# Performance work log

Measured on AMD Instinct MI355X. Metric: run time of the kernel, lower is better.

## Reference

```python
import jax, jax.numpy as jnp
import numpy as np

NQ, NS, D, NUM_CLASSES = 8192, 16384, 512, 64


def setup_inputs() -> dict:
    key = jax.random.key(0)
    k1, k2, k3 = jax.random.split(key, 3)
    query_embeddings = jax.random.normal(k1, (NQ, D), dtype=jnp.float32)
    support_embeddings = jax.random.normal(k2, (NS, D), dtype=jnp.float32)
    # one-hot support labels [NS, NUM_CLASSES]
    labels = jax.random.randint(k3, (NS,), 0, NUM_CLASSES)
    support_labels_onehot = jax.nn.one_hot(labels, NUM_CLASSES, dtype=jnp.float32)
    return {
        "query_embeddings": query_embeddings,
        "support_embeddings": support_embeddings,
        "support_labels_onehot": support_labels_onehot,
    }


def reference(query_embeddings, support_embeddings, support_labels_onehot):
    """KNNLearner.predict_prob with distance_type='cosine'.

    distance = -cos_sim(query, support)          [NQ, NS]
    top-1 over (-distance) -> nearest support, value = max similarity
    gather support label, one-hot, scale by value. [NQ, NUM_CLASSES]
    """
    eps = 1e-12  # tf.nn.l2_normalize epsilon guard
    q = query_embeddings * jax.lax.rsqrt(
        jnp.maximum(jnp.sum(query_embeddings * query_embeddings, axis=1, keepdims=True), eps))
    s = support_embeddings * jax.lax.rsqrt(
        jnp.maximum(jnp.sum(support_embeddings * support_embeddings, axis=1, keepdims=True), eps))
    distance = -jnp.einsum('qd,sd->qs', q, s)  # [NQ, NS]
    values, indices = jax.lax.top_k(-distance, 1)  # [NQ,1], similarity of nearest neighbor
    indices = indices[:, 0]
    values = values[:, 0]
    labels_x = jnp.argmax(support_labels_onehot, axis=1)  # [NS]
    labels_pred = labels_x[indices]  # [NQ]
    num_classes = support_labels_onehot.shape[1]
    labels_onehot = jax.nn.one_hot(labels_pred, num_classes, dtype=values.dtype)
    labels_prob = labels_onehot * values[:, None]  # [NQ, NUM_CLASSES]
    return labels_prob
```

## Files before the change

### kernel.cpp

```cpp
#include <hip/hip_runtime.h>
#include <stdint.h>

#define NQ 8192
#define NS 16384
#define DIM 512
#define NC 64
#define MARGIN 0.01f
#define CAND_CAP (1 << 20)
#define LCAP 1024

typedef unsigned short ushort;
typedef __attribute__((ext_vector_type(8))) short bf16x8;
typedef __attribute__((ext_vector_type(4))) float f32x4;

__device__ __forceinline__ uint32_t fkey(float f) {
  uint32_t u = __float_as_uint(f);
  return (u & 0x80000000u) ? ~u : (u | 0x80000000u);
}
__device__ __forceinline__ float unfkey(uint32_t k) {
  return __uint_as_float((k & 0x80000000u) ? (k & 0x7FFFFFFFu) : ~k);
}
__device__ __forceinline__ ushort f2bf_rne(float f) {
  uint32_t u = __float_as_uint(f);
  return (ushort)((u + 0x7fffu + ((u >> 16) & 1u)) >> 16);
}
__device__ __forceinline__ void gload_lds16(const void* g, void* lds) {
  __builtin_amdgcn_global_load_lds(
      (const __attribute__((address_space(1))) uint32_t*)g,
      (__attribute__((address_space(3))) uint32_t*)lds, 16, 0, 0);
}

__global__ void norm_bf16_kernel(const float* __restrict__ X,
                                 ushort* __restrict__ Xbf, float* __restrict__ rX,
                                 int nrows) {
  int w = threadIdx.x >> 6, l = threadIdx.x & 63;
  int row = blockIdx.x * 4 + w;
  if (row >= nrows) return;
  const float4* x = (const float4*)(X + (size_t)row * DIM);
  float4 v0 = x[l], v1 = x[l + 64];
  float s = v0.x*v0.x + v0.y*v0.y + v0.z*v0.z + v0.w*v0.w
          + v1.x*v1.x + v1.y*v1.y + v1.z*v1.z + v1.w*v1.w;
  #pragma unroll
  for (int off = 32; off; off >>= 1) s += __shfl_xor(s, off);
  float r = rsqrtf(fmaxf(s, 1e-12f));
  if (l == 0) rX[row] = r;
  size_t base = (size_t)row * DIM + 4 * l;
  *(ushort4*)&Xbf[base] = make_ushort4(f2bf_rne(v0.x*r), f2bf_rne(v0.y*r),
                                       f2bf_rne(v0.z*r), f2bf_rne(v0.w*r));
  *(ushort4*)&Xbf[base + 256] = make_ushort4(f2bf_rne(v1.x*r), f2bf_rne(v1.y*r),
                                             f2bf_rne(v1.z*r), f2bf_rne(v1.w*r));
}

__global__ void label_init_kernel(const float* __restrict__ oh, int* __restrict__ lab,
                                  unsigned long long* __restrict__ packedE,
                                  uint32_t* __restrict__ packedA, int* __restrict__ cnt) {
  int i = blockIdx.x * 256 + threadIdx.x;
  if (i == 0) *cnt = 0;
  if (i < NQ) { packedE[i] = 0ull; packedA[i] = 0u; }
  if (i < NS) {
    const float* row = oh + (size_t)i * NC;
    int l = 0;
    #pragma unroll
    for (int j = 0; j < NC; ++j) l = (row[j] > 0.5f) ? j : l;
    lab[i] = l;
  }
}

__global__ __launch_bounds__(512, 2) void gemm_margin_kernel(
    const ushort* __restrict__ Qbf, const ushort* __restrict__ Sbf,
    uint32_t* __restrict__ packedA, int4* __restrict__ cand, int* __restrict__ cnt)
{
  __shared__ ushort Atile[2][128 * 64];
  __shared__ ushort Btile[2][256 * 64];
  __shared__ float merged[128][4];
  __shared__ float runmax[128];
  __shared__ int4 lbuf[LCAP];
  __shared__ int lcnt, lbase;

  const int tid = threadIdx.x;
  const int w = tid >> 6, l = tid & 63;
  const int wr = w >> 2, wcn = w & 3;
  const int c = l & 15, g = l >> 4;

  const int flat = blockIdx.x;
  const int nf = (flat & 7) * 128 + (flat >> 3);
  const int sbq = nf >> 6, qb = nf & 63;
  const int qbase = qb * 128, sbase = sbq * 1024;

  const int lrow = l >> 3;
  const size_t lslot = (size_t)(((l & 7) ^ lrow) * 16);
  const char* srcA = (const char*)Qbf + (size_t)(qbase + w * 8 + lrow) * 1024 + lslot;
  const char* srcB = (const char*)Sbf + (size_t)(sbase + w * 8 + lrow) * 1024 + lslot;
  const int ldst = (w * 8) * 128;

  #define STAGE_A(buf, ks1) do { const size_t kb_ = (size_t)(((ks1) & 7) * 128);       \
    gload_lds16(srcA + kb_,             (char*)&Atile[(buf)][0] + ldst);               \
    gload_lds16(srcA + kb_ + 64 * 1024, (char*)&Atile[(buf)][0] + ldst + 64 * 128);    \
  } while (0)
  #define STAGE_B(buf, ks1) do {                                                       \
    const size_t ob_ = (size_t)((ks1) >> 3) * 256 * 1024 + (size_t)(((ks1) & 7) * 128);\
    gload_lds16(srcB + ob_,              (char*)&Btile[(buf)][0] + ldst);              \
    gload_lds16(srcB + ob_ +  64 * 1024, (char*)&Btile[(buf)][0] + ldst +  64 * 128);  \
    gload_lds16(srcB + ob_ + 128 * 1024, (char*)&Btile[(buf)][0] + ldst + 128 * 128);  \
    gload_lds16(srcB + ob_ + 192 * 1024, (char*)&Btile[(buf)][0] + ldst + 192 * 128);  \
  } while (0)

  const int arow = (wr * 64 + c) * 128;
  const int brow = (wcn * 64 + c) * 128;
  const int sl0 = (g ^ (c & 7)) * 16;
  const int sl1 = ((4 + g) ^ (c & 7)) * 16;

  float rm = -2.0f;
  if (tid == 0) lcnt = 0;

  STAGE_A(0, 0); STAGE_B(0, 0);
  asm volatile("s_waitcnt vmcnt(0)" ::: "memory");
  __builtin_amdgcn_s_barrier();

  for (int t = 0; t < 4; ++t) {
    f32x4 acc[4][4];
    #pragma unroll
    for (int m = 0; m < 4; ++m)
      #pragma unroll
      for (int n = 0; n < 4; ++n) acc[m][n] = (f32x4)0.0f;

    for (int k8 = 0; k8 < 8; ++k8) {
      const int ks = t * 8 + k8;
      const int cur = ks & 1, nxt = cur ^ 1;
      const bool pf = (ks + 1 < 32);
      const char* At = (const char*)&Atile[cur][0];
      const char* Bt = (const char*)&Btile[cur][0];
      bf16x8 ah[4], bh[4];

      #pragma unroll
      for (int m = 0; m < 4; ++m) ah[m] = *(const bf16x8*)(At + arow + m * 16 * 128 + sl0);
      #pragma unroll
      for (int n = 0; n < 4; ++n) bh[n] = *(const bf16x8*)(Bt + brow + n * 16 * 128 + sl0);
      if (pf) STAGE_A(nxt, ks + 1);
      asm volatile("s_waitcnt lgkmcnt(0)" ::: "memory");
      __builtin_amdgcn_s_setprio(1);
      #pragma unroll
      for (int m = 0; m < 4; ++m)
        #pragma unroll
        for (int n = 0; n < 4; ++n)
          acc[m][n] = __builtin_amdgcn_mfma_f32_16x16x32_bf16(ah[m], bh[n], acc[m][n], 0, 0, 0);
      __builtin_amdgcn_s_setprio(0);

      #pragma unroll
      for (int m = 0; m < 4; ++m) ah[m] = *(const bf16x8*)(At + arow + m * 16 * 128 + sl1);
      #pragma unroll
      for (int n = 0; n < 4; ++n) bh[n] = *(const bf16x8*)(Bt + brow + n * 16 * 128 + sl1);
      if (pf) STAGE_B(nxt, ks + 1);
      asm volatile("s_waitcnt lgkmcnt(0)" ::: "memory");
      __builtin_amdgcn_s_setprio(1);
      #pragma unroll
      for (int m = 0; m < 4; ++m)
        #pragma unroll
        for (int n = 0; n < 4; ++n)
          acc[m][n] = __builtin_amdgcn_mfma_f32_16x16x32_bf16(ah[m], bh[n], acc[m][n], 0, 0, 0);
      __builtin_amdgcn_s_setprio(0);

      asm volatile("s_waitcnt vmcnt(0)" ::: "memory");
      __builtin_amdgcn_s_barrier();
    }

    #pragma unroll
    for (int m = 0; m < 4; ++m)
      #pragma unroll
      for (int r = 0; r < 4; ++r) {
        float v = acc[m][0][r];
        #pragma unroll
        for (int j = 1; j < 4; ++j) v = fmaxf(v, acc[m][j][r]);
        #pragma unroll
        for (int off = 1; off < 16; off <<= 1) v = fmaxf(v, __shfl_xor(v, off));
        if (c == 0) merged[wr * 64 + m * 16 + g * 4 + r][wcn] = v;
      }
    __syncthreads();
    if (tid < 128) {
      float tmax = fmaxf(fmaxf(merged[tid][0], merged[tid][1]),
                         fmaxf(merged[tid][2], merged[tid][3]));
      rm = fmaxf(rm, tmax);
      runmax[tid] = rm;
    }
    __syncthreads();
    {
      const int sb = sbase + t * 256 + wcn * 64 + c;
      #pragma unroll
      for (int m = 0; m < 4; ++m)
        #pragma unroll
        for (int r = 0; r < 4; ++r) {
          const int row = wr * 64 + m * 16 + g * 4 + r;
          const float thr = runmax[row] - MARGIN;
          #pragma unroll
          for (int j = 0; j < 4; ++j) {
            float v = acc[m][j][r];
            if (v >= thr) {
              int s = atomicAdd(&lcnt, 1);
              if (s < LCAP)
                lbuf[s] = make_int4(qbase + row, sb + j * 16, __float_as_int(v), 0);
            }
          }
        }
    }
    __syncthreads();
    if (tid == 0) {
      int take = lcnt < LCAP ? lcnt : LCAP;
      lbase = atomicAdd(cnt, take);
      lcnt = take;
    }
    __syncthreads();
    for (int i = tid; i < lcnt; i += 512) {
      int gi = lbase + i;
      if (gi < CAND_CAP) cand[gi] = lbuf[i];
    }
    __syncthreads();
    if (tid == 0) lcnt = 0;
  }

  if (tid < 128) atomicMax(&packedA[qbase + tid], fkey(rm));

  #undef STAGE_A
  #undef STAGE_B
}

__global__ void rescore_kernel(const float* __restrict__ Q, const float* __restrict__ S,
                               const float* __restrict__ rq, const float* __restrict__ rs,
                               const uint32_t* __restrict__ packedA,
                               const int4* __restrict__ cand, const int* __restrict__ cnt,
                               unsigned long long* __restrict__ packedE) {
  const int nw = (gridDim.x * blockDim.x) >> 6;
  const int wid = (blockIdx.x * blockDim.x + threadIdx.x) >> 6;
  const int l = threadIdx.x & 63;
  int n = *cnt; if (n > CAND_CAP) n = CAND_CAP;
  for (int ci = wid; ci < n; ci += nw) {
    int4 cd = cand[ci];
    float maxA = unfkey(packedA[cd.x]);
    float apx = __int_as_float(cd.z);
    if (apx < maxA - MARGIN) continue;
    const float4* qp = (const float4*)(Q + (size_t)cd.x * DIM);
    const float4* sp = (const float4*)(S + (size_t)cd.y * DIM);
    float4 a0 = qp[l], b0 = sp[l], a1 = qp[l + 64], b1 = sp[l + 64];
    float d = a0.x*b0.x + a0.y*b0.y + a0.z*b0.z + a0.w*b0.w
            + a1.x*b1.x + a1.y*b1.y + a1.z*b1.z + a1.w*b1.w;
    #pragma unroll
    for (int off = 32; off; off >>= 1) d += __shfl_xor(d, off);
    if (l == 0) {
      float ex = d * rq[cd.x] * rs[cd.y];
      unsigned long long p =
          ((unsigned long long)fkey(ex) << 32) | (uint32_t)(~(uint32_t)cd.y);
      atomicMax(&packedE[cd.x], p);
    }
  }
}

__global__ void finalize_kernel(const unsigned long long* __restrict__ packedE,
                                const int* __restrict__ lab, float* __restrict__ out) {
  int gid = blockIdx.x * 256 + threadIdx.x;
  if (gid >= NQ * NC) return;
  int q = gid >> 6, cl = gid & 63;
  unsigned long long p = packedE[q];
  if (p == 0ull) { out[gid] = 0.0f; return; }
  uint32_t n = ~(uint32_t)p;
  float v = unfkey((uint32_t)(p >> 32));
  out[gid] = (cl == lab[n]) ? v : 0.0f;
}

extern "C" void kernel_launch(void* const* d_in, const int* in_sizes, int n_in,
                              void* d_out, int out_size, void* d_ws, size_t ws_size,
                              hipStream_t stream) {
  const float* Q  = (const float*)d_in[0];
  const float* S  = (const float*)d_in[1];
  const float* OH = (const float*)d_in[2];
  float* out = (float*)d_out;

  char* ws = (char*)d_ws;
  int* lab                    = (int*)(ws);
  unsigned long long* packedE = (unsigned long long*)(ws + (1 << 16));
  uint32_t* packedA           = (uint32_t*)(ws + (2 << 16));
  int* cnt                    = (int*)(ws + (3 << 16));
  float* rq                   = (float*)(ws + 200704);
  float* rs                   = (float*)(ws + 233472);
  ushort* Qbf                 = (ushort*)(ws + 299008);
  ushort* Sbf                 = (ushort*)(ws + 299008 + 8388608);
  int4* cand                  = (int4*)(ws + 299008 + 8388608 + 16777216);

  norm_bf16_kernel<<<NQ / 4, 256, 0, stream>>>(Q, Qbf, rq, NQ);
  norm_bf16_kernel<<<NS / 4, 256, 0, stream>>>(S, Sbf, rs, NS);
  label_init_kernel<<<NS / 256, 256, 0, stream>>>(OH, lab, packedE, packedA, cnt);

  gemm_margin_kernel<<<1024, 512, 0, stream>>>(Qbf, Sbf, packedA, cand, cnt);

  rescore_kernel<<<2048, 256, 0, stream>>>(Q, S, rq, rs, packedA, cand, cnt, packedE);

  finalize_kernel<<<(NQ * NC) / 256, 256, 0, stream>>>(packedE, lab, out);
}
```

Measured before the change: 302.0 us.

## Enlarge GEMM tile to 256x256 with triple-buffered BK=32 pipeline

Reworks the similarity GEMM to use 256x256 output tiles with a K step of 32, a three-stage LDS ring buffer and a prefetch distance of two steps, waiting only on older loads (vmcnt(4)). The S dimension is split into 8 chunks, giving 256 blocks at one block per CU. Each wave now computes 8x4 MFMA tiles, which raises arithmetic intensity and cuts LDS and global traffic per FLOP. In exchange it uses more registers and LDS, halves occupancy and grid size (256 blocks may underfill the device), adds an extra barrier per tile, and enlarges the local candidate buffer.

```diff
diff --git a/kernel.cpp b/kernel.cpp
--- a/kernel.cpp
+++ b/kernel.cpp
@@ -7,7 +7,16 @@
 #define NC 64
 #define MARGIN 0.01f
 #define CAND_CAP (1 << 20)
-#define LCAP 1024
+#define LCAP 2048
+
+#define BM 256
+#define BN 256
+#define BK 32
+#define SSPLIT 8
+#define SCHUNK (NS / SSPLIT)
+#define NTILES (SCHUNK / BN)
+#define KSTEPS (DIM / BK)
+#define TOTKS (NTILES * KSTEPS)
 
 typedef unsigned short ushort;
 typedef __attribute__((ext_vector_type(8))) short bf16x8;
@@ -66,14 +75,13 @@
   }
 }
 
-__global__ __launch_bounds__(512, 2) void gemm_margin_kernel(
+__global__ __launch_bounds__(512, 1) void gemm_margin_kernel(
     const ushort* __restrict__ Qbf, const ushort* __restrict__ Sbf,
     uint32_t* __restrict__ packedA, int4* __restrict__ cand, int* __restrict__ cnt)
 {
-  __shared__ ushort Atile[2][128 * 64];
-  __shared__ ushort Btile[2][256 * 64];
-  __shared__ float merged[128][4];
-  __shared__ float runmax[128];
+  __shared__ ushort tiles[3][2][BM * BK];
+  __shared__ float merged[BM][4];
+  __shared__ float runmax[BM];
   __shared__ int4 lbuf[LCAP];
   __shared__ int lcnt, lbase;
 
@@ -83,89 +91,74 @@
   const int c = l & 15, g = l >> 4;
 
   const int flat = blockIdx.x;
-  const int nf = (flat & 7) * 128 + (flat >> 3);
-  const int sbq = nf >> 6, qb = nf & 63;
-  const int qbase = qb * 128, sbase = sbq * 1024;
-
-  const int lrow = l >> 3;
-  const size_t lslot = (size_t)(((l & 7) ^ lrow) * 16);
-  const char* srcA = (const char*)Qbf + (size_t)(qbase + w * 8 + lrow) * 1024 + lslot;
-  const char* srcB = (const char*)Sbf + (size_t)(sbase + w * 8 + lrow) * 1024 + lslot;
-  const int ldst = (w * 8) * 128;
-
-  #define STAGE_A(buf, ks1) do { const size_t kb_ = (size_t)(((ks1) & 7) * 128);       \
-    gload_lds16(srcA + kb_,             (char*)&Atile[(buf)][0] + ldst);               \
-    gload_lds16(srcA + kb_ + 64 * 1024, (char*)&Atile[(buf)][0] + ldst + 64 * 128);    \
+  const int nf = (flat & 7) * 32 + (flat >> 3);
+  const int sbq = nf >> 5, qb = nf & 31;
+  const int qbase = qb * BM, sbase = sbq * SCHUNK;
+
+  const int lrow = l >> 2;
+  const int lslot = ((l & 3) ^ (lrow & 3)) * 16;
+  const char* srcA0 = (const char*)Qbf + (size_t)(qbase + w * 32 + lrow) * 1024 + lslot;
+  const char* srcB0 = (const char*)Sbf + (size_t)(sbase + w * 32 + lrow) * 1024 + lslot;
+  const int ldst0 = (w * 32) * 64;
+
+  #define STAGE(n) do {                                                         \
+    const int nb_ = (n) % 3;                                                    \
+    const int kb_ = ((n) & (KSTEPS - 1)) * 64;                                  \
+    const size_t ob_ = (size_t)((n) >> 4) * (BN * 1024) + kb_;                  \
+    char* at_ = (char*)&tiles[nb_][0][0];                                       \
+    char* bt_ = (char*)&tiles[nb_][1][0];                                       \
+    gload_lds16(srcA0 + kb_,         at_ + ldst0);                              \
+    gload_lds16(srcA0 + kb_ + 16384, at_ + ldst0 + 1024);                       \
+    gload_lds16(srcB0 + ob_,         bt_ + ldst0);                              \
+    gload_lds16(srcB0 + ob_ + 16384, bt_ + ldst0 + 1024);                       \
   } while (0)
-  #define STAGE_B(buf, ks1) do {                                                       \
-    const size_t ob_ = (size_t)((ks1) >> 3) * 256 * 1024 + (size_t)(((ks1) & 7) * 128);\
-    gload_lds16(srcB + ob_,              (char*)&Btile[(buf)][0] + ldst);              \
-    gload_lds16(srcB + ob_ +  64 * 1024, (char*)&Btile[(buf)][0] + ldst +  64 * 128);  \
-    gload_lds16(srcB + ob_ + 128 * 1024, (char*)&Btile[(buf)][0] + ldst + 128 * 128);  \
-    gload_lds16(srcB + ob_ + 192 * 1024, (char*)&Btile[(buf)][0] + ldst + 192 * 128);  \
-  } while (0)
-
-  const int arow = (wr * 64 + c) * 128;
-  const int brow = (wcn * 64 + c) * 128;
-  const int sl0 = (g ^ (c & 7)) * 16;
-  const int sl1 = ((4 + g) ^ (c & 7)) * 16;
+
+  const int slot = (g ^ (c & 3)) * 16;
+  const int aoff = (wr * 128 + c) * 64 + slot;
+  const int boff = (wcn * 64 + c) * 64 + slot;
 
   float rm = -2.0f;
   if (tid == 0) lcnt = 0;
 
-  STAGE_A(0, 0); STAGE_B(0, 0);
-  asm volatile("s_waitcnt vmcnt(0)" ::: "memory");
+  STAGE(0); STAGE(1);
+  asm volatile("s_waitcnt vmcnt(4)" ::: "memory");
   __builtin_amdgcn_s_barrier();
 
-  for (int t = 0; t < 4; ++t) {
-    f32x4 acc[4][4];
-    #pragma unroll
-    for (int m = 0; m < 4; ++m)
+  for (int t = 0; t < NTILES; ++t) {
+    f32x4 acc[8][4];
+    #pragma unroll
+    for (int m = 0; m < 8; ++m)
       #pragma unroll
       for (int n = 0; n < 4; ++n) acc[m][n] = (f32x4)0.0f;
 
-    for (int k8 = 0; k8 < 8; ++k8) {
-      const int ks = t * 8 + k8;
-      const int cur = ks & 1, nxt = cur ^ 1;
-      const bool pf = (ks + 1 < 32);
-      const char* At = (const char*)&Atile[cur][0];
-      const char* Bt = (const char*)&Btile[cur][0];
-      bf16x8 ah[4], bh[4];
-
-      #pragma unroll
-      for (int m = 0; m < 4; ++m) ah[m] = *(const bf16x8*)(At + arow + m * 16 * 128 + sl0);
-      #pragma unroll
-      for (int n = 0; n < 4; ++n) bh[n] = *(const bf16x8*)(Bt + brow + n * 16 * 128 + sl0);
-      if (pf) STAGE_A(nxt, ks + 1);
-      asm volatile("s_waitcnt lgkmcnt(0)" ::: "memory");
+    for (int k16 = 0; k16 < KSTEPS; ++k16) {
+      const int n = t * KSTEPS + k16;
+      const int cur = n % 3;
+      const char* At = (const char*)&tiles[cur][0][0];
+      const char* Bt = (const char*)&tiles[cur][1][0];
+
+      bf16x8 ah[8], bh[4];
+      #pragma unroll
+      for (int m = 0; m < 8; ++m) ah[m] = *(const bf16x8*)(At + aoff + m * 1024);
+      #pragma unroll
+      for (int j = 0; j < 4; ++j) bh[j] = *(const bf16x8*)(Bt + boff + j * 1024);
+
+      if (n + 2 < TOTKS) STAGE(n + 2);
+
       __builtin_amdgcn_s_setprio(1);
       #pragma unroll
-      for (int m = 0; m < 4; ++m)
-        #pragma unroll
-        for (int n = 0; n < 4; ++n)
-          acc[m][n] = __builtin_amdgcn_mfma_f32_16x16x32_bf16(ah[m], bh[n], acc[m][n], 0, 0, 0);
+      for (int m = 0; m < 8; ++m)
+        #pragma unroll
+        for (int j = 0; j < 4; ++j)
+          acc[m][j] = __builtin_amdgcn_mfma_f32_16x16x32_bf16(ah[m], bh[j], acc[m][j], 0, 0, 0);
       __builtin_amdgcn_s_setprio(0);
 
-      #pragma unroll
-      for (int m = 0; m < 4; ++m) ah[m] = *(const bf16x8*)(At + arow + m * 16 * 128 + sl1);
-      #pragma unroll
-      for (int n = 0; n < 4; ++n) bh[n] = *(const bf16x8*)(Bt + brow + n * 16 * 128 + sl1);
-      if (pf) STAGE_B(nxt, ks + 1);
-      asm volatile("s_waitcnt lgkmcnt(0)" ::: "memory");
-      __builtin_amdgcn_s_setprio(1);
-      #pragma unroll
-      for (int m = 0; m < 4; ++m)
-        #pragma unroll
-        for (int n = 0; n < 4; ++n)
-          acc[m][n] = __builtin_amdgcn_mfma_f32_16x16x32_bf16(ah[m], bh[n], acc[m][n], 0, 0, 0);
-      __builtin_amdgcn_s_setprio(0);
-
-      asm volatile("s_waitcnt vmcnt(0)" ::: "memory");
+      asm volatile("s_waitcnt vmcnt(4)" ::: "memory");
       __builtin_amdgcn_s_barrier();
     }
 
     #pragma unroll
-    for (int m = 0; m < 4; ++m)
+    for (int m = 0; m < 8; ++m)
       #pragma unroll
       for (int r = 0; r < 4; ++r) {
         float v = acc[m][0][r];
@@ -173,10 +166,10 @@
         for (int j = 1; j < 4; ++j) v = fmaxf(v, acc[m][j][r]);
         #pragma unroll
         for (int off = 1; off < 16; off <<= 1) v = fmaxf(v, __shfl_xor(v, off));
-        if (c == 0) merged[wr * 64 + m * 16 + g * 4 + r][wcn] = v;
+        if (c == 0) merged[wr * 128 + m * 16 + g * 4 + r][wcn] = v;
       }
     __syncthreads();
-    if (tid < 128) {
+    if (tid < BM) {
       float tmax = fmaxf(fmaxf(merged[tid][0], merged[tid][1]),
                          fmaxf(merged[tid][2], merged[tid][3]));
       rm = fmaxf(rm, tmax);
@@ -184,12 +177,12 @@
     }
     __syncthreads();
     {
-      const int sb = sbase + t * 256 + wcn * 64 + c;
-      #pragma unroll
-      for (int m = 0; m < 4; ++m)
+      const int sb = sbase + t * BN + wcn * 64 + c;
+      #pragma unroll
+      for (int m = 0; m < 8; ++m)
         #pragma unroll
         for (int r = 0; r < 4; ++r) {
-          const int row = wr * 64 + m * 16 + g * 4 + r;
+          const int row = wr * 128 + m * 16 + g * 4 + r;
           const float thr = runmax[row] - MARGIN;
           #pragma unroll
           for (int j = 0; j < 4; ++j) {
@@ -215,12 +208,12 @@
     }
     __syncthreads();
     if (tid == 0) lcnt = 0;
+    __syncthreads();
   }
 
-  if (tid < 128) atomicMax(&packedA[qbase + tid], fkey(rm));
-
-  #undef STAGE_A
-  #undef STAGE_B
+  if (tid < BM) atomicMax(&packedA[qbase + tid], fkey(rm));
+
+  #undef STAGE
 }
 
 __global__ void rescore_kernel(const float* __restrict__ Q, const float* __restrict__ S,
@@ -288,7 +281,7 @@
   norm_bf16_kernel<<<NS / 4, 256, 0, stream>>>(S, Sbf, rs, NS);
   label_init_kernel<<<NS / 256, 256, 0, stream>>>(OH, lab, packedE, packedA, cnt);
 
-  gemm_margin_kernel<<<1024, 512, 0, stream>>>(Qbf, Sbf, packedA, cand, cnt);
+  gemm_margin_kernel<<<(NQ / BM) * SSPLIT, 512, 0, stream>>>(Qbf, Sbf, packedA, cand, cnt);
 
   rescore_kernel<<<2048, 256, 0, stream>>>(Q, S, rq, rs, packedA, cand, cnt, packedE);
 
```

Result: faster. 290.3 us (-3.9%).

## Triple-buffer GEMM LDS tiles with two-stage prefetch and spill overflow candidates

Applied to the files above, without the earlier changes.

Moves the bf16 GEMM main loop from double to triple buffering of the A/B LDS tiles. It prefetches two k-steps ahead and waits with vmcnt(6) instead of draining all loads each step. LCAP is halved to keep LDS within budget, and candidates that overflow the local buffer now go straight to the global list instead of being dropped. A barrier is also added after resetting the local counter. The deeper pipeline uses more LDS, which could limit occupancy at 2 blocks per CU.

```diff
diff --git a/kernel.cpp b/kernel.cpp
--- a/kernel.cpp
+++ b/kernel.cpp
@@ -7,7 +7,7 @@
 #define NC 64
 #define MARGIN 0.01f
 #define CAND_CAP (1 << 20)
-#define LCAP 1024
+#define LCAP 512
 
 typedef unsigned short ushort;
 typedef __attribute__((ext_vector_type(8))) short bf16x8;
@@ -70,8 +70,8 @@
     const ushort* __restrict__ Qbf, const ushort* __restrict__ Sbf,
     uint32_t* __restrict__ packedA, int4* __restrict__ cand, int* __restrict__ cnt)
 {
-  __shared__ ushort Atile[2][128 * 64];
-  __shared__ ushort Btile[2][256 * 64];
+  __shared__ ushort Atile[3][128 * 64];
+  __shared__ ushort Btile[3][256 * 64];
   __shared__ float merged[128][4];
   __shared__ float runmax[128];
   __shared__ int4 lbuf[LCAP];
@@ -93,28 +93,29 @@
   const char* srcB = (const char*)Sbf + (size_t)(sbase + w * 8 + lrow) * 1024 + lslot;
   const int ldst = (w * 8) * 128;
 
-  #define STAGE_A(buf, ks1) do { const size_t kb_ = (size_t)(((ks1) & 7) * 128);       \
-    gload_lds16(srcA + kb_,             (char*)&Atile[(buf)][0] + ldst);               \
-    gload_lds16(srcA + kb_ + 64 * 1024, (char*)&Atile[(buf)][0] + ldst + 64 * 128);    \
+  #define STAGE_A(buf, n) do { const size_t kb_ = (size_t)((n) & 7) * 128;          \
+    gload_lds16(srcA + kb_,         (char*)&Atile[(buf)][0] + ldst);                \
+    gload_lds16(srcA + kb_ + 65536, (char*)&Atile[(buf)][0] + ldst + 8192);         \
   } while (0)
-  #define STAGE_B(buf, ks1) do {                                                       \
-    const size_t ob_ = (size_t)((ks1) >> 3) * 256 * 1024 + (size_t)(((ks1) & 7) * 128);\
-    gload_lds16(srcB + ob_,              (char*)&Btile[(buf)][0] + ldst);              \
-    gload_lds16(srcB + ob_ +  64 * 1024, (char*)&Btile[(buf)][0] + ldst +  64 * 128);  \
-    gload_lds16(srcB + ob_ + 128 * 1024, (char*)&Btile[(buf)][0] + ldst + 128 * 128);  \
-    gload_lds16(srcB + ob_ + 192 * 1024, (char*)&Btile[(buf)][0] + ldst + 192 * 128);  \
+  #define STAGE_B(buf, n) do {                                                      \
+    const size_t ob_ = (size_t)((n) >> 3) * 262144 + (size_t)((n) & 7) * 128;       \
+    gload_lds16(srcB + ob_,          (char*)&Btile[(buf)][0] + ldst);               \
+    gload_lds16(srcB + ob_ +  65536, (char*)&Btile[(buf)][0] + ldst +  8192);       \
+    gload_lds16(srcB + ob_ + 131072, (char*)&Btile[(buf)][0] + ldst + 16384);       \
+    gload_lds16(srcB + ob_ + 196608, (char*)&Btile[(buf)][0] + ldst + 24576);       \
   } while (0)
 
   const int arow = (wr * 64 + c) * 128;
   const int brow = (wcn * 64 + c) * 128;
-  const int sl0 = (g ^ (c & 7)) * 16;
+  const int sl0 = ((g) ^ (c & 7)) * 16;
   const int sl1 = ((4 + g) ^ (c & 7)) * 16;
 
   float rm = -2.0f;
   if (tid == 0) lcnt = 0;
 
   STAGE_A(0, 0); STAGE_B(0, 0);
-  asm volatile("s_waitcnt vmcnt(0)" ::: "memory");
+  STAGE_A(1, 1); STAGE_B(1, 1);
+  asm volatile("s_waitcnt vmcnt(6)" ::: "memory");
   __builtin_amdgcn_s_barrier();
 
   for (int t = 0; t < 4; ++t) {
@@ -125,9 +126,10 @@
       for (int n = 0; n < 4; ++n) acc[m][n] = (f32x4)0.0f;
 
     for (int k8 = 0; k8 < 8; ++k8) {
-      const int ks = t * 8 + k8;
-      const int cur = ks & 1, nxt = cur ^ 1;
-      const bool pf = (ks + 1 < 32);
+      const int n = t * 8 + k8;
+      const int cur = n % 3;
+      const int pre = (n + 2) % 3;
+      const bool pf = (n + 2 < 32);
       const char* At = (const char*)&Atile[cur][0];
       const char* Bt = (const char*)&Btile[cur][0];
       bf16x8 ah[4], bh[4];
@@ -135,32 +137,33 @@
       #pragma unroll
       for (int m = 0; m < 4; ++m) ah[m] = *(const bf16x8*)(At + arow + m * 16 * 128 + sl0);
       #pragma unroll
-      for (int n = 0; n < 4; ++n) bh[n] = *(const bf16x8*)(Bt + brow + n * 16 * 128 + sl0);
-      if (pf) STAGE_A(nxt, ks + 1);
+      for (int j = 0; j < 4; ++j) bh[j] = *(const bf16x8*)(Bt + brow + j * 16 * 128 + sl0);
+      if (pf) STAGE_A(pre, n + 2);
       asm volatile("s_waitcnt lgkmcnt(0)" ::: "memory");
       __builtin_amdgcn_s_setprio(1);
       #pragma unroll
       for (int m = 0; m < 4; ++m)
         #pragma unroll
-        for (int n = 0; n < 4; ++n)
-          acc[m][n] = __builtin_amdgcn_mfma_f32_16x16x32_bf16(ah[m], bh[n], acc[m][n], 0, 0, 0);
+        for (int j = 0; j < 4; ++j)
+          acc[m][j] = __builtin_amdgcn_mfma_f32_16x16x32_bf16(ah[m], bh[j], acc[m][j], 0, 0, 0);
       __builtin_amdgcn_s_setprio(0);
 
       #pragma unroll
       for (int m = 0; m < 4; ++m) ah[m] = *(const bf16x8*)(At + arow + m * 16 * 128 + sl1);
       #pragma unroll
-      for (int n = 0; n < 4; ++n) bh[n] = *(const bf16x8*)(Bt + brow + n * 16 * 128 + sl1);
-      if (pf) STAGE_B(nxt, ks + 1);
+      for (int j = 0; j < 4; ++j) bh[j] = *(const bf16x8*)(Bt + brow + j * 16 * 128 + sl1);
+      if (pf) STAGE_B(pre, n + 2);
       asm volatile("s_waitcnt lgkmcnt(0)" ::: "memory");
       __builtin_amdgcn_s_setprio(1);
       #pragma unroll
       for (int m = 0; m < 4; ++m)
         #pragma unroll
-        for (int n = 0; n < 4; ++n)
-          acc[m][n] = __builtin_amdgcn_mfma_f32_16x16x32_bf16(ah[m], bh[n], acc[m][n], 0, 0, 0);
+        for (int j = 0; j < 4; ++j)
+          acc[m][j] = __builtin_amdgcn_mfma_f32_16x16x32_bf16(ah[m], bh[j], acc[m][j], 0, 0, 0);
       __builtin_amdgcn_s_setprio(0);
 
-      asm volatile("s_waitcnt vmcnt(0)" ::: "memory");
+      if (pf) asm volatile("s_waitcnt vmcnt(6)" ::: "memory");
+      else    asm volatile("s_waitcnt vmcnt(0)" ::: "memory");
       __builtin_amdgcn_s_barrier();
     }
 
@@ -196,8 +199,11 @@
             float v = acc[m][j][r];
             if (v >= thr) {
               int s = atomicAdd(&lcnt, 1);
-              if (s < LCAP)
-                lbuf[s] = make_int4(qbase + row, sb + j * 16, __float_as_int(v), 0);
+              if (s < LCAP) lbuf[s] = make_int4(qbase + row, sb + j * 16, __float_as_int(v), 0);
+              else {
+                int gi = atomicAdd(cnt, 1);
+                if (gi < CAND_CAP) cand[gi] = make_int4(qbase + row, sb + j * 16, __float_as_int(v), 0);
+              }
             }
           }
         }
@@ -215,6 +221,7 @@
     }
     __syncthreads();
     if (tid == 0) lcnt = 0;
+    __syncthreads();
   }
 
   if (tid < 128) atomicMax(&packedA[qbase + tid], fkey(rm));
```

Result: no change. 297.5 us (-1.5%).
